# Optimization experiments

Hardware: AMD Instinct MI355X
Metric: run time of the kernel (lower is better)

The kernel has to match this reference:

```python
import jax, jax.numpy as jnp
import numpy as np
import math

B, T, C = 64, 1024, 12
D, H, L = 512, 8, 2
FFN = 4 * D
FC_HIDDEN, NUM_CLASSES = 256, 5
KERNEL = 25          # config.moving_average default
FACTOR = 3           # config.autocorrelation_factor default
TOP_K = int(FACTOR * math.log(T))
EPS = 1e-5
MIN_SCALE = 1e-10


def _sinusoidal_pos(n_pos, dim):
    # HF AutoformerSinusoidalPositionalEmbedding._init_weight (Marian-style: sin block then cos block)
    pos = np.arange(n_pos, dtype=np.float64)[:, None]
    j = np.arange(dim)[None, :]
    enc = pos / np.power(10000.0, 2 * (j // 2) / dim)
    half = dim // 2
    out = np.zeros((n_pos, dim), np.float32)
    out[:, :half] = np.sin(enc[:, 0::2])
    out[:, half:] = np.cos(enc[:, 1::2])
    return jnp.asarray(out)


def _layernorm(x, g, b):
    mu = jnp.mean(x, axis=-1, keepdims=True)
    var = jnp.mean(jnp.square(x - mu), axis=-1, keepdims=True)
    return (x - mu) * jax.lax.rsqrt(var + EPS) * g + b


def _series_decomp_seasonal(x):
    # moving-average trend with edge-replication padding; return seasonal = x - trend
    pad = (KERNEL - 1) // 2
    xp = jnp.pad(x, ((0, 0), (pad, pad), (0, 0)), mode='edge')
    cs = jnp.cumsum(xp, axis=1)
    cs = jnp.concatenate([jnp.zeros_like(cs[:, :1]), cs], axis=1)
    trend = (cs[:, KERNEL:] - cs[:, :-KERNEL]) / KERNEL
    return x - trend


def _autocorr_attention(h, w, b):
    # w: (4, D, D) q/k/v/out, b: (4, D). Eval-mode HF AutoformerAttention (per-batch delays).
    hd = D // H
    def split(t):
        return t.reshape(B, T, H, hd).transpose(0, 2, 1, 3)  # (B,H,T,hd)
    q = split(h @ w[0] + b[0])
    k = split(h @ w[1] + b[1])
    v = split(h @ w[2] + b[2])
    # period-based dependency discovery via FFT cross-correlation along time
    qf = jnp.fft.rfft(q, n=T, axis=2)
    kf = jnp.fft.rfft(k, n=T, axis=2)
    corr = jnp.fft.irfft(qf * jnp.conj(kf), n=T, axis=2)  # (B,H,T,hd)
    mean_corr = corr.mean(axis=(1, 3))                    # (B,T)
    top_vals, top_idx = jax.lax.top_k(mean_corr, TOP_K)   # (B,K)
    wts = jax.nn.softmax(top_vals, axis=-1)               # (B,K)
    t_idx = jnp.arange(T)
    agg = jnp.zeros_like(v)
    for i in range(TOP_K):  # small fixed K, mirrors HF loop; circular roll by -delay
        idx = (t_idx[None, :] + top_idx[:, i][:, None]) % T      # (B,T)
        rolled = jnp.take_along_axis(v, idx[:, None, :, None], axis=2)
        agg = agg + rolled * wts[:, i][:, None, None, None]
    out = agg.transpose(0, 2, 1, 3).reshape(B, T, D)
    return out @ w[3] + b[3]


def _forward(x, emb_w, emb_ln_g, emb_ln_b, attn_w, attn_b, ln_g, ln_b,
             fc1_w, fc1_b, fc2_w, fc2_b, head_w1, head_b1, head_w2, head_b2):
    # AutoformerMeanScaler (observed mask is all-ones): scale = mean |x| over time, loc = 0
    scale = jnp.clip(jnp.mean(jnp.abs(x), axis=1, keepdims=True), MIN_SCALE)  # (B,1,C)
    inputs = x / scale
    # static features: log1p(|loc|)=0 and log(scale), broadcast over time; lags=[0] -> lagged == inputs
    static = jnp.concatenate([jnp.zeros_like(scale), jnp.log(scale)], axis=-1)  # (B,1,2C)
    feats = jnp.broadcast_to(static, (B, T, 2 * C))
    ti = jnp.concatenate([inputs, feats], axis=-1)  # (B,T,3C)

    h = ti @ emb_w + _sinusoidal_pos(T, D)[None]
    h = _layernorm(h, emb_ln_g, emb_ln_b)

    for l in range(L):
        res = h
        a = _autocorr_attention(h, attn_w[l], attn_b[l])
        h = _layernorm(res + a, ln_g[l, 0], ln_b[l, 0])
        h = _series_decomp_seasonal(h)
        res = h
        f = jax.nn.gelu(h @ fc1_w[l] + fc1_b[l], approximate=False)
        h = res + f @ fc2_w[l] + fc2_b[l]
        h = _layernorm(h, ln_g[l, 1], ln_b[l, 1])
        h = _series_decomp_seasonal(h)

    feat = h.mean(axis=1)  # (B,D)
    return jax.nn.relu(feat @ head_w1 + head_b1) @ head_w2 + head_b2  # (B,num_classes)


def setup_inputs() -> dict:
    key = jax.random.key(0)
    ks = jax.random.split(key, 8)
    s = 0.02
    rn = lambda k, shape: jax.random.normal(k, shape, jnp.float32) * s
    return {
        'x': jax.random.normal(ks[0], (B, T, C), jnp.float32),
        'emb_w': rn(ks[1], (3 * C, D)),
        'emb_ln_g': jnp.ones((D,), jnp.float32),
        'emb_ln_b': jnp.zeros((D,), jnp.float32),
        'attn_w': rn(ks[2], (L, 4, D, D)),
        'attn_b': jnp.zeros((L, 4, D), jnp.float32),
        'ln_g': jnp.ones((L, 2, D), jnp.float32),
        'ln_b': jnp.zeros((L, 2, D), jnp.float32),
        'fc1_w': rn(ks[3], (L, D, FFN)),
        'fc1_b': jnp.zeros((L, FFN), jnp.float32),
        'fc2_w': rn(ks[4], (L, FFN, D)),
        'fc2_b': jnp.zeros((L, D), jnp.float32),
        'head_w1': rn(ks[5], (D, FC_HIDDEN)),
        'head_b1': jnp.zeros((FC_HIDDEN,), jnp.float32),
        'head_w2': rn(ks[6], (FC_HIDDEN, NUM_CLASSES)),
        'head_b2': jnp.zeros((NUM_CLASSES,), jnp.float32),
    }


def reference(x, emb_w, emb_ln_g, emb_ln_b, attn_w, attn_b, ln_g, ln_b,
              fc1_w, fc1_b, fc2_w, fc2_b, head_w1, head_b1, head_w2, head_b2):
    return _forward(x, emb_w, emb_ln_g, emb_ln_b, attn_w, attn_b, ln_g, ln_b,
                    fc1_w, fc1_b, fc2_w, fc2_b, head_w1, head_b1, head_w2, head_b2)
```

## Files before the change

### kernel.cpp

```cpp
#include <hip/hip_runtime.h>
#include <math.h>

#define CB 64
#define CT 1024
#define CCH 12
#define CD 512
#define CL 2
#define CFFN 2048
#define CFCH 256
#define CNC 5
#define CTOPK 20
#define CEPS 1e-5f

typedef __attribute__((ext_vector_type(8))) short bfrag;
typedef __attribute__((ext_vector_type(4))) float ffrag;

__device__ inline ushort bf16r(float f) {
  unsigned u = __float_as_uint(f);
  unsigned r = (u + 0x7FFFu + ((u >> 16) & 1u)) >> 16;
  return (ushort)r;
}
__device__ inline float bf16f(ushort h) { return __uint_as_float(((unsigned)h) << 16); }

__device__ __forceinline__ void gld16(const ushort* g, ushort* l) {
  __builtin_amdgcn_global_load_lds((__attribute__((address_space(1))) void*)g,
                                   (__attribute__((address_space(3))) void*)l,
                                   16, 0, 0);
}

struct c32 { float x, y; };
__device__ inline c32 cadd(c32 a, c32 b) { return c32{a.x + b.x, a.y + b.y}; }
__device__ inline c32 csub(c32 a, c32 b) { return c32{a.x - b.x, a.y - b.y}; }
__device__ inline c32 cmul(c32 a, c32 b) {
  return c32{a.x * b.x - a.y * b.y, a.x * b.y + a.y * b.x};
}
__device__ inline c32 cmulj(c32 a, c32 b) {
  return c32{a.x * b.x + a.y * b.y, a.y * b.x - a.x * b.y};
}
__device__ inline c32 mineg_i(c32 a) { return c32{a.y, -a.x}; }
__device__ inline c32 mul_i(c32 a) { return c32{-a.y, a.x}; }

#define ZIDX(p) ((p) + ((p) >> 4))

__device__ inline int drev4(int t) {
  return ((t & 3) << 8) | (((t >> 2) & 3) << 6) | (((t >> 4) & 3) << 4) |
         (((t >> 6) & 3) << 2) | ((t >> 8) & 3);
}

template <int INV>
__device__ inline void fft_stage(c32* zz, const c32* twl, int tid, int s) {
  int L = 1 << (2 * s);
  int j = tid & (L - 1);
  int g = tid >> (2 * s);
  int p0 = (g << (2 * s + 2)) + j;
  int tb = j << (8 - 2 * s);
  c32 w1 = twl[ZIDX(tb)], w2 = twl[ZIDX(2 * tb)], w3 = twl[ZIDX(3 * tb)];
  c32 b0 = zz[ZIDX(p0)], b1 = zz[ZIDX(p0 + L)], b2 = zz[ZIDX(p0 + 2 * L)],
      b3 = zz[ZIDX(p0 + 3 * L)];
  if (INV) { b1 = cmulj(b1, w1); b2 = cmulj(b2, w2); b3 = cmulj(b3, w3); }
  else     { b1 = cmul(b1, w1);  b2 = cmul(b2, w2);  b3 = cmul(b3, w3); }
  c32 e0 = cadd(b0, b2), e1 = csub(b0, b2), e2 = cadd(b1, b3), e3 = csub(b1, b3);
  c32 e3r = INV ? mul_i(e3) : mineg_i(e3);
  zz[ZIDX(p0)] = cadd(e0, e2);
  zz[ZIDX(p0 + L)] = cadd(e1, e3r);
  zz[ZIDX(p0 + 2 * L)] = csub(e0, e2);
  zz[ZIDX(p0 + 3 * L)] = csub(e1, e3r);
}

__device__ inline void unp_acc(const c32* zf, int w, c32& acc) {
  int wc = (1024 - w) & 1023;
  c32 Z1 = zf[ZIDX(w)];
  c32 Z2r = zf[ZIDX(wc)];
  c32 Z2 = c32{Z2r.x, -Z2r.y};
  c32 Qf = c32{0.5f * (Z1.x + Z2.x), 0.5f * (Z1.y + Z2.y)};
  c32 M = c32{Z1.x - Z2.x, Z1.y - Z2.y};
  c32 Kf = c32{0.5f * M.y, -0.5f * M.x};
  acc.x += Qf.x * Kf.x + Qf.y * Kf.y;
  acc.y += Qf.y * Kf.x - Qf.x * Kf.y;
}

__global__ __launch_bounds__(256) void k_twid(c32* __restrict__ tw) {
  int j = blockIdx.x * 256 + threadIdx.x;
  double a = -2.0 * 3.14159265358979323846 * (double)j / 1024.0;
  tw[j] = c32{(float)cos(a), (float)sin(a)};
}

__global__ __launch_bounds__(256) void k_scale(const float* __restrict__ x,
                                               float* __restrict__ sc,
                                               float* __restrict__ lg) {
  int b = blockIdx.x, tid = threadIdx.x;
  float acc[CCH];
#pragma unroll
  for (int c = 0; c < CCH; ++c) acc[c] = 0.f;
  const float* xb = x + (size_t)b * CT * CCH;
  for (int t = tid; t < CT; t += 256) {
    const float* row = xb + t * CCH;
#pragma unroll
    for (int c = 0; c < CCH; ++c) acc[c] += fabsf(row[c]);
  }
  __shared__ float red[256][CCH];
#pragma unroll
  for (int c = 0; c < CCH; ++c) red[tid][c] = acc[c];
  __syncthreads();
  for (int off = 128; off > 0; off >>= 1) {
    if (tid < off) {
#pragma unroll
      for (int c = 0; c < CCH; ++c) red[tid][c] += red[tid + off][c];
    }
    __syncthreads();
  }
  if (tid < CCH) {
    float s = fmaxf(red[0][tid] * (1.0f / CT), 1e-10f);
    sc[b * CCH + tid] = s;
    lg[b * CCH + tid] = logf(s);
  }
}

__global__ __launch_bounds__(512) void k_postab(float* __restrict__ pos) {
  int t = blockIdx.x;
  int d = threadIdx.x;
  double v;
  if (d < 256) {
    double w = pow(10000.0, -((double)d) / 256.0);
    v = sin((double)t * w);
  } else {
    double w = pow(10000.0, -((double)(d - 256)) / 256.0);
    v = cos((double)t * w);
  }
  pos[(size_t)t * CD + d] = (float)v;
}

__global__ __launch_bounds__(128) void k_embed(const float* __restrict__ x,
                                               const float* __restrict__ sc,
                                               const float* __restrict__ lg,
                                               const float* __restrict__ W,
                                               const float* __restrict__ postab,
                                               const float* __restrict__ g,
                                               const float* __restrict__ beta,
                                               float* __restrict__ h,
                                               ushort* __restrict__ h2) {
  int row = blockIdx.x;
  int b = row >> 10, t = row & 1023;
  int tid = threadIdx.x;
  __shared__ float xs[CCH], ls[CCH];
  if (tid < CCH) {
    float s = sc[b * CCH + tid];
    xs[tid] = x[(size_t)row * CCH + tid] / s;
    ls[tid] = lg[b * CCH + tid];
  }
  __syncthreads();
  int d0 = tid * 4;
  float4 p = *(const float4*)(postab + (size_t)t * CD + d0);
  float v0 = p.x, v1 = p.y, v2 = p.z, v3 = p.w;
#pragma unroll
  for (int c = 0; c < CCH; ++c) {
    float xc = xs[c], lc = ls[c];
    float4 w0 = *(const float4*)(W + (size_t)c * CD + d0);
    float4 w1 = *(const float4*)(W + (size_t)(24 + c) * CD + d0);
    v0 += xc * w0.x + lc * w1.x;
    v1 += xc * w0.y + lc * w1.y;
    v2 += xc * w0.z + lc * w1.z;
    v3 += xc * w0.w + lc * w1.w;
  }
  float s1 = v0 + v1 + v2 + v3;
  float s2 = v0 * v0 + v1 * v1 + v2 * v2 + v3 * v3;
  for (int off = 32; off > 0; off >>= 1) {
    s1 += __shfl_down(s1, off);
    s2 += __shfl_down(s2, off);
  }
  __shared__ float ws1[2], ws2[2], mv[2];
  int wid = tid >> 6, lane = tid & 63;
  if (lane == 0) { ws1[wid] = s1; ws2[wid] = s2; }
  __syncthreads();
  if (tid == 0) {
    float S1 = ws1[0] + ws1[1], S2 = ws2[0] + ws2[1];
    float mu = S1 * (1.0f / CD);
    float var = S2 * (1.0f / CD) - mu * mu;
    mv[0] = mu;
    mv[1] = 1.0f / sqrtf(var + CEPS);
  }
  __syncthreads();
  float mu = mv[0], ri = mv[1];
  float4 gg = *(const float4*)(g + d0);
  float4 bb = *(const float4*)(beta + d0);
  float4 o;
  o.x = (v0 - mu) * ri * gg.x + bb.x;
  o.y = (v1 - mu) * ri * gg.y + bb.y;
  o.z = (v2 - mu) * ri * gg.z + bb.z;
  o.w = (v3 - mu) * ri * gg.w + bb.w;
  *(float4*)(h + (size_t)row * CD + d0) = o;
  ushort4 hv = {bf16r(o.x), bf16r(o.y), bf16r(o.z), bf16r(o.w)};
  *(ushort4*)(h2 + (size_t)row * CD + d0) = hv;
}

__global__ __launch_bounds__(256) void k_cvtw(const float* __restrict__ W,
                                              ushort* __restrict__ W2,
                                              int K, int N) {
  __shared__ float tile[32][33];
  int tx = threadIdx.x & 31, ty = threadIdx.x >> 5;
  int n0 = blockIdx.x * 32, k0 = blockIdx.y * 32;
#pragma unroll
  for (int r = 0; r < 4; ++r)
    tile[ty * 4 + r][tx] = W[(size_t)(k0 + ty * 4 + r) * N + n0 + tx];
  __syncthreads();
#pragma unroll
  for (int r = 0; r < 4; ++r) {
    int nl = ty * 4 + r, kl = tx;
    W2[(size_t)(n0 + nl) * K + k0 + kl] = bf16r(tile[kl][nl]);
  }
}

template <int EPI>
__global__ __launch_bounds__(256) void k_gemm3(const ushort* __restrict__ A,
                                               const ushort* __restrict__ W,
                                               const float* __restrict__ bias,
                                               const float* __restrict__ R,
                                               float* __restrict__ Cf,
                                               ushort* __restrict__ Cs,
                                               ushort* __restrict__ Cs2,
                                               int lda, int ldb, int ldc, int K) {
  __shared__ ushort AhS[3][128 * 32];
  __shared__ ushort BhS[3][128 * 32];
  int tid = threadIdx.x;
  int nx = gridDim.x;
  int nwg = nx * gridDim.y;
  int flat = blockIdx.y * nx + blockIdx.x;
  int sw = (flat & 7) * (nwg >> 3) + (flat >> 3);
  int n0 = (sw % nx) * 128, m0 = (sw / nx) * 128;
  int wid = __builtin_amdgcn_readfirstlane(tid >> 6);
  int lane = tid & 63;
  int lr = lane >> 2;
  int lc = ((lane & 3) ^ ((lr >> 2) & 3)) * 8;
  int wm = wid >> 1, wn = wid & 1;
  int mOff = wm * 64, nOff = wn * 64;
  int quad = lane >> 4, l16 = lane & 15;

  const ushort* pA = A + (size_t)(m0 + wid * 32 + lr) * lda + lc;
  const ushort* pB = W + (size_t)(n0 + wid * 32 + lr) * ldb + lc;
  const int NK = K >> 5;

  ffrag acc[4][4];
#pragma unroll
  for (int i = 0; i < 4; ++i)
#pragma unroll
    for (int j = 0; j < 4; ++j) acc[i][j] = (ffrag)(0.f);

#define ISSUE(t, buf)                                                        \
  {                                                                          \
    int kk = (t) << 5;                                                       \
    ushort* lA = &AhS[buf][(wid * 32) * 32];                                 \
    ushort* lB = &BhS[buf][(wid * 32) * 32];                                 \
    gld16(pA + kk, lA);                                                      \
    gld16(pA + (size_t)16 * lda + kk, lA + 16 * 32);                         \
    gld16(pB + kk, lB);                                                      \
    gld16(pB + (size_t)16 * ldb + kk, lB + 16 * 32);                         \
  }

  ISSUE(0, 0);
  ISSUE(1, 1);
  ISSUE(2, 2);
  for (int k = 0; k < NK; ++k) {
    if (k + 2 < NK) {
      asm volatile("s_waitcnt vmcnt(8)\n\ts_barrier" ::: "memory");
    } else if (k + 1 < NK) {
      asm volatile("s_waitcnt vmcnt(4)\n\ts_barrier" ::: "memory");
    } else {
      asm volatile("s_waitcnt vmcnt(0)\n\ts_barrier" ::: "memory");
    }
    int buf = k % 3;
    bfrag ah[4], bh[4];
#pragma unroll
    for (int i = 0; i < 4; ++i) {
      int row = mOff + i * 16 + l16;
      ah[i] = *(const bfrag*)&AhS[buf][row * 32 + (quad ^ ((row >> 2) & 3)) * 8];
    }
#pragma unroll
    for (int j = 0; j < 4; ++j) {
      int row = nOff + j * 16 + l16;
      bh[j] = *(const bfrag*)&BhS[buf][row * 32 + (quad ^ ((row >> 2) & 3)) * 8];
    }
#pragma unroll
    for (int i = 0; i < 4; ++i)
#pragma unroll
      for (int j = 0; j < 4; ++j)
        acc[i][j] = __builtin_amdgcn_mfma_f32_16x16x32_bf16(ah[i], bh[j], acc[i][j], 0, 0, 0);
    asm volatile("s_barrier" ::: "memory");
    if (k + 3 < NK) ISSUE(k + 3, (k + 3) % 3);
  }
#undef ISSUE

#pragma unroll
  for (int j = 0; j < 4; ++j) {
    int col = n0 + nOff + j * 16 + l16;
    float bcol = bias[col];
#pragma unroll
    for (int i = 0; i < 4; ++i) {
      int rowb = m0 + mOff + i * 16 + quad * 4;
      if (EPI == 7) {
        if (col < 1024) {
          float4 o = {acc[i][j][0] + bcol, acc[i][j][1] + bcol,
                      acc[i][j][2] + bcol, acc[i][j][3] + bcol};
          *(float4*)(Cf + (size_t)col * ldc + rowb) = o;
        } else {
          float* Vf = (float*)Cs;
#pragma unroll
          for (int r = 0; r < 4; ++r)
            Vf[(size_t)(rowb + r) * 512 + (col - 1024)] = acc[i][j][r] + bcol;
        }
      } else {
#pragma unroll
        for (int r = 0; r < 4; ++r) {
          int row = rowb + r;
          float vv = acc[i][j][r] + bcol;
          if (EPI == 1) vv = 0.5f * vv * (1.0f + erff(vv * 0.7071067811865475f));
          if (EPI == 2) vv += R[(size_t)row * ldc + col];
          if (EPI == 1) {
            Cs[(size_t)row * ldc + col] = bf16r(vv);
          } else {
            Cf[(size_t)row * ldc + col] = vv;
          }
        }
      }
    }
  }
}

__global__ __launch_bounds__(256) void k_fft(const float* __restrict__ QT,
                                             const c32* __restrict__ twg,
                                             c32* __restrict__ part, int Mc) {
  __shared__ c32 z[4][1088];
  __shared__ c32 twl[1088];
  int dg = blockIdx.x, zb = blockIdx.y, tid = threadIdx.x;
#pragma unroll
  for (int k = 0; k < 4; ++k) {
    int i = tid + k * 256;
    twl[ZIDX(i)] = twg[i];
  }
  c32 pa = {0.f, 0.f}, pb = {0.f, 0.f}, p5 = {0.f, 0.f};
  for (int i = 0; i < 4; ++i) {
    int d0 = dg * 16 + i * 4;
#pragma unroll
    for (int f = 0; f < 4; ++f) {
      const float* qr = QT + (size_t)(d0 + f) * Mc + (size_t)zb * 1024;
      const float* kr = QT + (size_t)(512 + d0 + f) * Mc + (size_t)zb * 1024;
#pragma unroll
      for (int k = 0; k < 4; ++k) {
        int t = tid + k * 256;
        z[f][ZIDX(drev4(t))] = c32{qr[t], kr[t]};
      }
    }
    __syncthreads();
    for (int s = 0; s < 5; ++s) {
#pragma unroll
      for (int f = 0; f < 4; ++f) fft_stage<0>(&z[f][0], twl, tid, s);
      __syncthreads();
    }
#pragma unroll
    for (int f = 0; f < 4; ++f) {
      unp_acc(&z[f][0], tid, pa);
      unp_acc(&z[f][0], tid + 256, pb);
      if (tid == 0) unp_acc(&z[f][0], 512, p5);
    }
    __syncthreads();
  }
  c32* po = part + ((size_t)zb * 32 + dg) * 513;
  po[tid] = pa;
  po[tid + 256] = pb;
  if (tid == 0) po[512] = p5;
}

__global__ __launch_bounds__(256) void k_spectopk(const c32* __restrict__ part,
                                                  const c32* __restrict__ twg,
                                                  float* __restrict__ wts,
                                                  int* __restrict__ idxs) {
  int b = blockIdx.x, tid = threadIdx.x;
  __shared__ c32 twl[1088];
  __shared__ c32 S[1024];
  __shared__ c32 zz[1088];
  __shared__ float corr[1024];
#pragma unroll
  for (int k = 0; k < 4; ++k) {
    int i = tid + k * 256;
    twl[ZIDX(i)] = twg[i];
  }
  c32 sa = {0.f, 0.f}, sb = {0.f, 0.f}, s5 = {0.f, 0.f};
  const c32* pbase = part + (size_t)b * 32 * 513;
  for (int p = 0; p < 32; ++p) {
    const c32* pp = pbase + p * 513;
    sa = cadd(sa, pp[tid]);
    sb = cadd(sb, pp[tid + 256]);
    if (tid == 0) s5 = cadd(s5, pp[512]);
  }
  S[tid] = sa;
  S[tid + 256] = sb;
  if (tid == 0) S[512] = s5;
  if (tid > 0) S[1024 - tid] = c32{sa.x, -sa.y};
  S[768 - tid] = c32{sb.x, -sb.y};
  __syncthreads();
#pragma unroll
  for (int k = 0; k < 4; ++k) {
    int t = tid + k * 256;
    zz[ZIDX(drev4(t))] = S[t];
  }
  __syncthreads();
  for (int s = 0; s < 5; ++s) {
    fft_stage<1>(&zz[0], twl, tid, s);
    __syncthreads();
  }
  const float scl = 1.0f / (1024.0f * 512.0f);
#pragma unroll
  for (int k = 0; k < 4; ++k) {
    int t = tid + k * 256;
    corr[t] = zz[ZIDX(t)].x * scl;
  }
  __syncthreads();
  __shared__ float swv[4];
  __shared__ int swi[4];
  __shared__ float selv[CTOPK];
  __shared__ int seli[CTOPK];
  int wid = tid >> 6, lane = tid & 63;
  for (int k = 0; k < CTOPK; ++k) {
    float bv = -INFINITY;
    int bi = 0;
#pragma unroll
    for (int q = 0; q < 4; ++q) {
      int idx = tid + q * 256;
      float v = corr[idx];
      if (v > bv || (v == bv && idx < bi)) { bv = v; bi = idx; }
    }
#pragma unroll
    for (int off = 32; off > 0; off >>= 1) {
      float ov = __shfl_down(bv, off);
      int oi = __shfl_down(bi, off);
      if (ov > bv || (ov == bv && oi < bi)) { bv = ov; bi = oi; }
    }
    if (lane == 0) { swv[wid] = bv; swi[wid] = bi; }
    __syncthreads();
    if (tid == 0) {
      float mvv = swv[0];
      int mi = swi[0];
      for (int q2 = 1; q2 < 4; ++q2)
        if (swv[q2] > mvv || (swv[q2] == mvv && swi[q2] < mi)) { mvv = swv[q2]; mi = swi[q2]; }
      selv[k] = mvv;
      seli[k] = mi;
      corr[mi] = -INFINITY;
    }
    __syncthreads();
  }
  if (tid == 0) {
    float mx = selv[0], sum = 0.f, e[CTOPK];
    for (int k = 0; k < CTOPK; ++k) {
      e[k] = expf(selv[k] - mx);
      sum += e[k];
    }
    float inv = 1.0f / sum;
    for (int k = 0; k < CTOPK; ++k) {
      wts[b * CTOPK + k] = e[k] * inv;
      idxs[b * CTOPK + k] = seli[k];
    }
  }
}

__global__ __launch_bounds__(128) void k_agg(const float* __restrict__ Vf,
                                             const float* __restrict__ wts,
                                             const int* __restrict__ idxs,
                                             ushort* __restrict__ out2) {
  int nb = gridDim.x;
  int blk = blockIdx.x;
  int row = (blk & 7) * (nb >> 3) + (blk >> 3);
  int b = row >> 10, t = row & 1023;
  int d0 = threadIdx.x * 4;
  const float* Vb = Vf + (size_t)b * CT * 512;
  float4 acc = {0.f, 0.f, 0.f, 0.f};
#pragma unroll
  for (int k = 0; k < CTOPK; ++k) {
    float w = wts[b * CTOPK + k];
    int r = t + idxs[b * CTOPK + k];
    if (r >= CT) r -= CT;
    float4 v = *(const float4*)(Vb + (size_t)r * 512 + d0);
    acc.x += w * v.x;
    acc.y += w * v.y;
    acc.z += w * v.z;
    acc.w += w * v.w;
  }
  ushort4 hv = {bf16r(acc.x), bf16r(acc.y), bf16r(acc.z), bf16r(acc.w)};
  *(ushort4*)(out2 + (size_t)row * CD + d0) = hv;
}

__global__ __launch_bounds__(128) void k_stats(const float* __restrict__ X,
                                               c32* __restrict__ st) {
  int row = blockIdx.x, tid = threadIdx.x;
  int d0 = tid * 4;
  float4 v = *(const float4*)(X + (size_t)row * CD + d0);
  float s1 = v.x + v.y + v.z + v.w;
  float s2 = v.x * v.x + v.y * v.y + v.z * v.z + v.w * v.w;
  for (int off = 32; off > 0; off >>= 1) {
    s1 += __shfl_down(s1, off);
    s2 += __shfl_down(s2, off);
  }
  __shared__ float ws1[2], ws2[2];
  int wid = tid >> 6, lane = tid & 63;
  if (lane == 0) { ws1[wid] = s1; ws2[wid] = s2; }
  __syncthreads();
  if (tid == 0) {
    float S1 = ws1[0] + ws1[1], S2 = ws2[0] + ws2[1];
    float mu = S1 * (1.0f / CD);
    float var = S2 * (1.0f / CD) - mu * mu;
    st[row] = c32{mu, 1.0f / sqrtf(var + CEPS)};
  }
}

__global__ __launch_bounds__(128) void k_dec2(const float* __restrict__ X,
                                              const c32* __restrict__ st,
                                              const float* __restrict__ g,
                                              float* __restrict__ out,
                                              ushort* __restrict__ out2) {
  int nb = gridDim.x;
  int blk = blockIdx.x;
  int row = (blk & 7) * (nb >> 3) + (blk >> 3);
  int b = row >> 10, t = row & 1023;
  int d0 = threadIdx.x * 4;
  const float* xb = X + (size_t)b * CT * CD + d0;
  const c32* sb = st + (size_t)b * CT;
  float4 s = {0.f, 0.f, 0.f, 0.f};
#pragma unroll
  for (int j = -12; j <= 12; ++j) {
    int tt = t + j;
    tt = tt < 0 ? 0 : (tt > CT - 1 ? CT - 1 : tt);
    c32 ms = sb[tt];
    float4 v = *(const float4*)(xb + (size_t)tt * CD);
    s.x += (v.x - ms.x) * ms.y;
    s.y += (v.y - ms.x) * ms.y;
    s.z += (v.z - ms.x) * ms.y;
    s.w += (v.w - ms.x) * ms.y;
  }
  c32 mc = sb[t];
  float4 xv = *(const float4*)(xb + (size_t)t * CD);
  float4 gg = *(const float4*)(g + d0);
  const float inv = 1.0f / 25.0f;
  float4 o;
  o.x = gg.x * ((xv.x - mc.x) * mc.y - s.x * inv);
  o.y = gg.y * ((xv.y - mc.x) * mc.y - s.y * inv);
  o.z = gg.z * ((xv.z - mc.x) * mc.y - s.z * inv);
  o.w = gg.w * ((xv.w - mc.x) * mc.y - s.w * inv);
  *(float4*)(out + (size_t)row * CD + d0) = o;
  ushort4 hv = {bf16r(o.x), bf16r(o.y), bf16r(o.z), bf16r(o.w)};
  *(ushort4*)(out2 + (size_t)row * CD + d0) = hv;
}

__global__ __launch_bounds__(256) void k_meanp(const float* __restrict__ X,
                                               float* __restrict__ part) {
  int b = blockIdx.x, g = blockIdx.y, tid = threadIdx.x;
  const float* xb = X + (size_t)b * CT * CD + (size_t)g * 128 * CD;
  float a0 = 0.f, a1 = 0.f;
  for (int r = 0; r < 128; ++r) {
    a0 += xb[(size_t)r * CD + tid];
    a1 += xb[(size_t)r * CD + tid + 256];
  }
  part[((size_t)b * 8 + g) * CD + tid] = a0;
  part[((size_t)b * 8 + g) * CD + tid + 256] = a1;
}

__global__ __launch_bounds__(256) void k_headf(const float* __restrict__ part,
                                               const float* __restrict__ w1,
                                               const float* __restrict__ b1,
                                               const float* __restrict__ w2,
                                               const float* __restrict__ b2,
                                               float* __restrict__ out) {
  int b = blockIdx.x, tid = threadIdx.x;
  __shared__ float f[CD];
  __shared__ float hid[CFCH];
  for (int d = tid; d < CD; d += 256) {
    float s = 0.f;
#pragma unroll
    for (int g = 0; g < 8; ++g) s += part[((size_t)b * 8 + g) * CD + d];
    f[d] = s * (1.0f / CT);
  }
  __syncthreads();
  float a = b1[tid];
  for (int d = 0; d < CD; ++d) a += f[d] * w1[d * CFCH + tid];
  hid[tid] = fmaxf(a, 0.f);
  __syncthreads();
  if (tid < CNC) {
    float a2 = b2[tid];
    for (int j = 0; j < CFCH; ++j) a2 += hid[j] * w2[j * CNC + tid];
    out[b * CNC + tid] = a2;
  }
}

extern "C" void kernel_launch(void* const* d_in, const int* in_sizes, int n_in,
                              void* d_out, int out_size, void* d_ws, size_t ws_size,
                              hipStream_t stream) {
  const float* x = (const float*)d_in[0];
  const float* emb_w = (const float*)d_in[1];
  const float* emb_g = (const float*)d_in[2];
  const float* emb_b = (const float*)d_in[3];
  const float* attn_w = (const float*)d_in[4];
  const float* attn_b = (const float*)d_in[5];
  const float* ln_g = (const float*)d_in[6];
  const float* ln_bb = (const float*)d_in[7];
  const float* fc1_w = (const float*)d_in[8];
  const float* fc1_b = (const float*)d_in[9];
  const float* fc2_w = (const float*)d_in[10];
  const float* fc2_b = (const float*)d_in[11];
  const float* hw1 = (const float*)d_in[12];
  const float* hb1 = (const float*)d_in[13];
  const float* hw2 = (const float*)d_in[14];
  const float* hb2 = (const float*)d_in[15];
  float* outp = (float*)d_out;

  const size_t WQ = 262144ULL;
  const size_t LW = 4 * WQ + 1048576ULL + 1048576ULL;
  const size_t W2TOT = CL * LW;

  const size_t FIXED_B = W2TOT * 2
                         + (size_t)CT * CD * 4
                         + 2 * (size_t)CB * CCH * 4
                         + 2 * (size_t)CB * CTOPK * 4
                         + (size_t)CB * 8 * CD * 4
                         + 1024 * 8
                         + 4096;
  const size_t PERB = 2ULL * CT * CD * 4 + (size_t)CT * CD * 2 + (size_t)CT * 2048 * 2 +
                      (size_t)32 * 513 * 8 + (size_t)CT * 8;
  int Bc = CB;
  while (Bc > 1) {
    if ((size_t)Bc * PERB + FIXED_B <= ws_size) break;
    Bc >>= 1;
  }
  const size_t CHF = (size_t)Bc * CT * CD;

  char* wsp = (char*)d_ws;
  float* P0 = (float*)wsp;     wsp += CHF * 4;
  float* P1 = (float*)wsp;     wsp += CHF * 4;
  ushort* U0 = (ushort*)wsp;   wsp += CHF * 2;
  ushort* U1 = (ushort*)wsp;   wsp += (size_t)Bc * CT * 2048 * 2;
  ushort* W2b = (ushort*)wsp;  wsp += W2TOT * 2;
  float* postab = (float*)wsp; wsp += (size_t)CT * CD * 4;
  float* scb = (float*)wsp;    wsp += (size_t)CB * CCH * 4;
  float* lgb = (float*)wsp;    wsp += (size_t)CB * CCH * 4;
  float* wtb = (float*)wsp;    wsp += (size_t)CB * CTOPK * 4;
  int* idb = (int*)wsp;        wsp += (size_t)CB * CTOPK * 4;
  float* partb = (float*)wsp;  wsp += (size_t)CB * 8 * CD * 4;
  c32* twc = (c32*)wsp;        wsp += 1024 * sizeof(c32);
  c32* partc = (c32*)wsp;      wsp += (size_t)Bc * 32 * 513 * sizeof(c32);
  c32* stb = (c32*)wsp;        wsp += (size_t)Bc * CT * sizeof(c32);

  for (int l = 0; l < CL; ++l) {
    ushort* wq2 = W2b + l * LW;
    ushort* wo2 = wq2 + 3 * WQ;
    ushort* w12 = wo2 + WQ;
    ushort* w22 = w12 + 1048576;
    for (int m = 0; m < 4; ++m)
      k_cvtw<<<dim3(CD / 32, CD / 32), 256, 0, stream>>>(
          attn_w + ((size_t)(l * 4 + m)) * CD * CD, wq2 + m * WQ, CD, CD);
    k_cvtw<<<dim3(CFFN / 32, CD / 32), 256, 0, stream>>>(
        fc1_w + (size_t)l * CD * CFFN, w12, CD, CFFN);
    k_cvtw<<<dim3(CD / 32, CFFN / 32), 256, 0, stream>>>(
        fc2_w + (size_t)l * CFFN * CD, w22, CFFN, CD);
  }

  k_scale<<<CB, 256, 0, stream>>>(x, scb, lgb);
  k_postab<<<CT, 512, 0, stream>>>(postab);
  k_twid<<<4, 256, 0, stream>>>(twc);

  for (int b0 = 0; b0 < CB; b0 += Bc) {
    const int Mc = Bc * CT;

    float* HP = P0;
    float* SA = P1;

    k_embed<<<Mc, 128, 0, stream>>>(x + (size_t)b0 * CT * CCH, scb + b0 * CCH,
                                    lgb + b0 * CCH, emb_w, postab, emb_g, emb_b,
                                    HP, U0);

    for (int l = 0; l < CL; ++l) {
      const float* bqkv = attn_b + (size_t)l * 4 * CD;
      const float* bo = attn_b + (size_t)(l * 4 + 3) * CD;
      const float* g0 = ln_g + (size_t)(l * 2 + 0) * CD;
      const float* g1 = ln_g + (size_t)(l * 2 + 1) * CD;
      const float* B1 = fc1_b + (size_t)l * CFFN;
      const float* B2f = fc2_b + (size_t)l * CD;
      const ushort* wq2 = W2b + l * LW;
      const ushort* wo2 = wq2 + 3 * WQ;
      const ushort* w12 = wo2 + WQ;
      const ushort* w22 = w12 + 1048576;

      k_gemm3<7><<<dim3(1536 / 128, Mc / 128), 256, 0, stream>>>(
          U0, wq2, bqkv, nullptr, (float*)U1, (ushort*)SA, nullptr, CD, CD, Mc, CD);
      k_fft<<<dim3(32, Bc), 256, 0, stream>>>((const float*)U1, twc, partc, Mc);
      k_spectopk<<<Bc, 256, 0, stream>>>(partc, twc, wtb, idb);
      k_agg<<<Mc, 128, 0, stream>>>((const float*)SA, wtb, idb, U0);
      k_gemm3<2><<<dim3(CD / 128, Mc / 128), 256, 0, stream>>>(
          U0, wo2, bo, HP, SA, nullptr, nullptr, CD, CD, CD, CD);
      k_stats<<<Mc, 128, 0, stream>>>(SA, stb);
      k_dec2<<<Mc, 128, 0, stream>>>(SA, stb, g0, HP, U0);
      k_gemm3<1><<<dim3(CFFN / 128, Mc / 128), 256, 0, stream>>>(
          U0, w12, B1, nullptr, nullptr, U1, nullptr, CD, CD, CFFN, CD);
      k_gemm3<2><<<dim3(CD / 128, Mc / 128), 256, 0, stream>>>(
          U1, w22, B2f, HP, SA, nullptr, nullptr, CFFN, CFFN, CD, CFFN);
      k_stats<<<Mc, 128, 0, stream>>>(SA, stb);
      k_dec2<<<Mc, 128, 0, stream>>>(SA, stb, g1, HP, U0);
    }

    k_meanp<<<dim3(Bc, 8), 256, 0, stream>>>(HP, partb + (size_t)b0 * 8 * CD);
    k_headf<<<Bc, 256, 0, stream>>>(partb + (size_t)b0 * 8 * CD, hw1, hb1, hw2, hb2,
                                    outp + (size_t)b0 * CNC);
  }
}
```

Baseline: 3.125 ms.

## Double-buffer GEMM, store V in bf16, and use a sliding-window decomposition kernel

Reduces the GEMM shared-memory pipeline from three stages to two. It also stores the V projection as bf16 instead of fp32, halving the bytes read by the top-k aggregation gather. The series-decomposition kernel is restructured so each block walks 64 consecutive timesteps with a running 25-tap window sum instead of re-reading 25 rows per output. Together these cut memory traffic and LDS usage, at the risk of less latency hiding in the GEMM and bf16 rounding of V.

```diff
diff --git a/kernel.cpp b/kernel.cpp
--- a/kernel.cpp
+++ b/kernel.cpp
@@ -219,8 +219,8 @@
                                                ushort* __restrict__ Cs,
                                                ushort* __restrict__ Cs2,
                                                int lda, int ldb, int ldc, int K) {
-  __shared__ ushort AhS[3][128 * 32];
-  __shared__ ushort BhS[3][128 * 32];
+  __shared__ ushort AhS[2][128 * 32];
+  __shared__ ushort BhS[2][128 * 32];
   int tid = threadIdx.x;
   int nx = gridDim.x;
   int nwg = nx * gridDim.y;
@@ -258,16 +258,13 @@
 
   ISSUE(0, 0);
   ISSUE(1, 1);
-  ISSUE(2, 2);
   for (int k = 0; k < NK; ++k) {
-    if (k + 2 < NK) {
-      asm volatile("s_waitcnt vmcnt(8)\n\ts_barrier" ::: "memory");
-    } else if (k + 1 < NK) {
+    if (k + 1 < NK) {
       asm volatile("s_waitcnt vmcnt(4)\n\ts_barrier" ::: "memory");
     } else {
       asm volatile("s_waitcnt vmcnt(0)\n\ts_barrier" ::: "memory");
     }
-    int buf = k % 3;
+    int buf = k & 1;
     bfrag ah[4], bh[4];
 #pragma unroll
     for (int i = 0; i < 4; ++i) {
@@ -285,7 +282,7 @@
       for (int j = 0; j < 4; ++j)
         acc[i][j] = __builtin_amdgcn_mfma_f32_16x16x32_bf16(ah[i], bh[j], acc[i][j], 0, 0, 0);
     asm volatile("s_barrier" ::: "memory");
-    if (k + 3 < NK) ISSUE(k + 3, (k + 3) % 3);
+    if (k + 2 < NK) ISSUE(k + 2, buf);
   }
 #undef ISSUE
 
@@ -302,10 +299,9 @@
                       acc[i][j][2] + bcol, acc[i][j][3] + bcol};
           *(float4*)(Cf + (size_t)col * ldc + rowb) = o;
         } else {
-          float* Vf = (float*)Cs;
 #pragma unroll
           for (int r = 0; r < 4; ++r)
-            Vf[(size_t)(rowb + r) * 512 + (col - 1024)] = acc[i][j][r] + bcol;
+            Cs[(size_t)(rowb + r) * 512 + (col - 1024)] = bf16r(acc[i][j][r] + bcol);
         }
       } else {
 #pragma unroll
@@ -461,7 +457,7 @@
   }
 }
 
-__global__ __launch_bounds__(128) void k_agg(const float* __restrict__ Vf,
+__global__ __launch_bounds__(128) void k_agg(const ushort* __restrict__ Vf,
                                              const float* __restrict__ wts,
                                              const int* __restrict__ idxs,
                                              ushort* __restrict__ out2) {
@@ -470,18 +466,18 @@
   int row = (blk & 7) * (nb >> 3) + (blk >> 3);
   int b = row >> 10, t = row & 1023;
   int d0 = threadIdx.x * 4;
-  const float* Vb = Vf + (size_t)b * CT * 512;
+  const ushort* Vb = Vf + (size_t)b * CT * 512;
   float4 acc = {0.f, 0.f, 0.f, 0.f};
 #pragma unroll
   for (int k = 0; k < CTOPK; ++k) {
     float w = wts[b * CTOPK + k];
     int r = t + idxs[b * CTOPK + k];
     if (r >= CT) r -= CT;
-    float4 v = *(const float4*)(Vb + (size_t)r * 512 + d0);
-    acc.x += w * v.x;
-    acc.y += w * v.y;
-    acc.z += w * v.z;
-    acc.w += w * v.w;
+    ushort4 v = *(const ushort4*)(Vb + (size_t)r * 512 + d0);
+    acc.x += w * bf16f(v.x);
+    acc.y += w * bf16f(v.y);
+    acc.z += w * bf16f(v.z);
+    acc.w += w * bf16f(v.w);
   }
   ushort4 hv = {bf16r(acc.x), bf16r(acc.y), bf16r(acc.z), bf16r(acc.w)};
   *(ushort4*)(out2 + (size_t)row * CD + d0) = hv;
@@ -510,42 +506,49 @@
   }
 }
 
-__global__ __launch_bounds__(128) void k_dec2(const float* __restrict__ X,
+__global__ __launch_bounds__(256) void k_dec2(const float* __restrict__ X,
                                               const c32* __restrict__ st,
                                               const float* __restrict__ g,
                                               float* __restrict__ out,
                                               ushort* __restrict__ out2) {
-  int nb = gridDim.x;
-  int blk = blockIdx.x;
-  int row = (blk & 7) * (nb >> 3) + (blk >> 3);
-  int b = row >> 10, t = row & 1023;
-  int d0 = threadIdx.x * 4;
-  const float* xb = X + (size_t)b * CT * CD + d0;
+  int b = blockIdx.y;
+  int t0 = blockIdx.x * 64;
+  int tid = threadIdx.x;
+  const float* xb = X + (size_t)b * CT * CD;
   const c32* sb = st + (size_t)b * CT;
-  float4 s = {0.f, 0.f, 0.f, 0.f};
+  float g0v = g[tid], g1v = g[tid + 256];
+  float s0 = 0.f, s1 = 0.f;
 #pragma unroll
   for (int j = -12; j <= 12; ++j) {
-    int tt = t + j;
-    tt = tt < 0 ? 0 : (tt > CT - 1 ? CT - 1 : tt);
-    c32 ms = sb[tt];
-    float4 v = *(const float4*)(xb + (size_t)tt * CD);
-    s.x += (v.x - ms.x) * ms.y;
-    s.y += (v.y - ms.x) * ms.y;
-    s.z += (v.z - ms.x) * ms.y;
-    s.w += (v.w - ms.x) * ms.y;
-  }
-  c32 mc = sb[t];
-  float4 xv = *(const float4*)(xb + (size_t)t * CD);
-  float4 gg = *(const float4*)(g + d0);
+    int u = t0 + j;
+    u = u < 0 ? 0 : (u > CT - 1 ? CT - 1 : u);
+    c32 ms = sb[u];
+    s0 += (xb[(size_t)u * CD + tid] - ms.x) * ms.y;
+    s1 += (xb[(size_t)u * CD + tid + 256] - ms.x) * ms.y;
+  }
   const float inv = 1.0f / 25.0f;
-  float4 o;
-  o.x = gg.x * ((xv.x - mc.x) * mc.y - s.x * inv);
-  o.y = gg.y * ((xv.y - mc.x) * mc.y - s.y * inv);
-  o.z = gg.z * ((xv.z - mc.x) * mc.y - s.z * inv);
-  o.w = gg.w * ((xv.w - mc.x) * mc.y - s.w * inv);
-  *(float4*)(out + (size_t)row * CD + d0) = o;
-  ushort4 hv = {bf16r(o.x), bf16r(o.y), bf16r(o.z), bf16r(o.w)};
-  *(ushort4*)(out2 + (size_t)row * CD + d0) = hv;
+  for (int tt = 0; tt < 64; ++tt) {
+    int t = t0 + tt;
+    c32 mc = sb[t];
+    float z0 = (xb[(size_t)t * CD + tid] - mc.x) * mc.y;
+    float z1 = (xb[(size_t)t * CD + tid + 256] - mc.x) * mc.y;
+    float o0 = g0v * (z0 - s0 * inv);
+    float o1 = g1v * (z1 - s1 * inv);
+    size_t ro = (size_t)(b * CT + t) * CD;
+    out[ro + tid] = o0;
+    out[ro + tid + 256] = o1;
+    out2[ro + tid] = bf16r(o0);
+    out2[ro + tid + 256] = bf16r(o1);
+    int ua = t + 13;
+    ua = ua > CT - 1 ? CT - 1 : ua;
+    int ur = t - 12;
+    ur = ur < 0 ? 0 : ur;
+    c32 ma = sb[ua], mr = sb[ur];
+    s0 += (xb[(size_t)ua * CD + tid] - ma.x) * ma.y -
+          (xb[(size_t)ur * CD + tid] - mr.x) * mr.y;
+    s1 += (xb[(size_t)ua * CD + tid + 256] - ma.x) * ma.y -
+          (xb[(size_t)ur * CD + tid + 256] - mr.x) * mr.y;
+  }
 }
 
 __global__ __launch_bounds__(256) void k_meanp(const float* __restrict__ X,
@@ -689,17 +692,17 @@
           U0, wq2, bqkv, nullptr, (float*)U1, (ushort*)SA, nullptr, CD, CD, Mc, CD);
       k_fft<<<dim3(32, Bc), 256, 0, stream>>>((const float*)U1, twc, partc, Mc);
       k_spectopk<<<Bc, 256, 0, stream>>>(partc, twc, wtb, idb);
-      k_agg<<<Mc, 128, 0, stream>>>((const float*)SA, wtb, idb, U0);
+      k_agg<<<Mc, 128, 0, stream>>>((const ushort*)SA, wtb, idb, U0);
       k_gemm3<2><<<dim3(CD / 128, Mc / 128), 256, 0, stream>>>(
-          U0, wo2, bo, HP, SA, nullptr, nullptr, CD, CD, CD, CD);
-      k_stats<<<Mc, 128, 0, stream>>>(SA, stb);
-      k_dec2<<<Mc, 128, 0, stream>>>(SA, stb, g0, HP, U0);
+          U0, wo2, bo, HP, (float*)SA, nullptr, nullptr, CD, CD, CD, CD);
+      k_stats<<<Mc, 128, 0, stream>>>((float*)SA, stb);
+      k_dec2<<<dim3(CT / 64, Bc), 256, 0, stream>>>((float*)SA, stb, g0, HP, U0);
       k_gemm3<1><<<dim3(CFFN / 128, Mc / 128), 256, 0, stream>>>(
           U0, w12, B1, nullptr, nullptr, U1, nullptr, CD, CD, CFFN, CD);
       k_gemm3<2><<<dim3(CD / 128, Mc / 128), 256, 0, stream>>>(
-          U1, w22, B2f, HP, SA, nullptr, nullptr, CFFN, CFFN, CD, CFFN);
-      k_stats<<<Mc, 128, 0, stream>>>(SA, stb);
-      k_dec2<<<Mc, 128, 0, stream>>>(SA, stb, g1, HP, U0);
+          U1, w22, B2f, HP, (float*)SA, nullptr, nullptr, CFFN, CFFN, CD, CFFN);
+      k_stats<<<Mc, 128, 0, stream>>>((float*)SA, stb);
+      k_dec2<<<dim3(CT / 64, Bc), 256, 0, stream>>>((float*)SA, stb, g1, HP, U0);
     }
 
     k_meanp<<<dim3(Bc, 8), 256, 0, stream>>>(HP, partb + (size_t)b0 * 8 * CD);
```

New measurement: 2.848 ms. -8.9%, faster.
